# Performance work log

Measured on AMD Instinct MI355X. Metric: run time of the kernel, lower is better.

## Reference

```python
import jax, jax.numpy as jnp
import numpy as np

V, E, H = 50000, 300, 512            # vocab, embed dim, rnn hidden
BS, NSEG, SLEN = 64, 3, 256          # batch, segments per sample (hardcoded 3), max seg len
NNODE, NFEAT, NHID, NOUT = 18, 600, 600, 1024  # GCN dims (hardcoded in module)


def _uniform(k, shape, stdv):
    return jax.random.uniform(k, shape, jnp.float32, -stdv, stdv)


def setup_inputs() -> dict:
    key = jax.random.key(0)
    ks = jax.random.split(key, 14)
    input_inds = jax.random.randint(ks[0], (BS, NSEG, SLEN), 0, V, dtype=jnp.int32)
    input_lens = jax.random.randint(ks[1], (BS, NSEG), 1, SLEN + 1, dtype=jnp.int32)
    emb = jax.random.normal(ks[2], (V, E), jnp.float32) * 0.1
    # GRU params (torch layout: [3H, in])
    sx = float(np.sqrt(6.0 / (3 * H + E)))
    sh = float(np.sqrt(6.0 / (3 * H + H)))
    w_ih = _uniform(ks[3], (3 * H, E), sx)
    w_hh = _uniform(ks[4], (3 * H, H), sh)
    b_ih = jnp.zeros((3 * H,), jnp.float32)
    b_hh = jnp.zeros((3 * H,), jnp.float32)
    # GCN params (uniform +-1/sqrt(out_features), per reset_parameters)
    s1 = 1.0 / float(np.sqrt(NHID))
    s2 = 1.0 / float(np.sqrt(NOUT))
    gw1 = _uniform(ks[5], (NFEAT, NHID), s1)
    gb1 = _uniform(ks[6], (NHID,), s1)
    gw2 = _uniform(ks[7], (NHID, NOUT), s2)
    gb2 = _uniform(ks[8], (NOUT,), s2)
    sg_x = jax.random.normal(ks[9], (BS, NNODE, NFEAT), jnp.float32)
    adj = jax.random.uniform(ks[10], (BS, NNODE, NNODE), jnp.float32)
    return dict(input_inds=input_inds, input_lens=input_lens, emb=emb,
                w_ih=w_ih, w_hh=w_hh, b_ih=b_ih, b_hh=b_hh,
                sg_x=sg_x, adj=adj, gw1=gw1, gb1=gb1, gw2=gw2, gb2=gb2)


def _gru(x, lens, w_ih, w_hh, b_ih, b_hh):
    """Length-masked batched GRU. x: [B,T,E], lens: [B]. Returns ys [B,T,H], hT [B,H]
    where hT equals the hidden state at the last valid step (carry frozen after len)."""
    B, T, _ = x.shape
    Hh = w_hh.shape[1]
    xi = jnp.einsum('bte,ge->btg', x, w_ih) + b_ih  # precompute input gates [B,T,3H]

    def step(h, inp):
        xi_t, t = inp
        gh = h @ w_hh.T + b_hh
        xr, xz, xn = jnp.split(xi_t, 3, axis=-1)
        hr, hz, hn = jnp.split(gh, 3, axis=-1)
        r = jax.nn.sigmoid(xr + hr)
        z = jax.nn.sigmoid(xz + hz)
        n = jnp.tanh(xn + r * hn)
        h_new = (1.0 - z) * n + z * h
        h_out = jnp.where((t < lens)[:, None], h_new, h)
        return h_out, h_out

    h0 = jnp.zeros((B, Hh), x.dtype)
    hT, ys = jax.lax.scan(step, h0, (jnp.swapaxes(xi, 0, 1), jnp.arange(T)))
    return jnp.swapaxes(ys, 0, 1), hT


def reference(input_inds, input_lens, emb, w_ih, w_hh, b_ih, b_hh,
              sg_x, adj, gw1, gb1, gw2, gb2):
    B3 = BS * NSEG
    T = NSEG * SLEN
    tok = emb[input_inds.reshape(B3, SLEN)]           # [B3, SLEN, E]
    ys, hT = _gru(tok, input_lens.reshape(B3), w_ih, w_hh, b_ih, b_hh)

    # Pack valid (segment, t) outputs contiguously per sample (the torch cat of
    # per-segment ragged outputs), pad tail with zeros.
    lens = input_lens                                            # [BS, NSEG]
    offs = jnp.concatenate([jnp.zeros((BS, 1), jnp.int32),
                            jnp.cumsum(lens, axis=1)[:, :-1]], axis=1)
    t_idx = jnp.arange(SLEN, dtype=jnp.int32)
    valid = t_idx[None, None, :] < lens[:, :, None]              # [BS, NSEG, SLEN]
    pos = jnp.where(valid, offs[:, :, None] + t_idx[None, None, :], T)
    pos = pos.reshape(BS, T)
    b_ix = jnp.arange(BS)[:, None]
    out_rfts = jnp.zeros((BS, T + 1, H), ys.dtype).at[b_ix, pos].set(
        ys.reshape(BS, T, H))[:, :T]
    out_embs = jnp.zeros((BS, T + 1, E), tok.dtype).at[b_ix, pos].set(
        tok.reshape(BS, T, E))[:, :T]
    tlen = jnp.sum(lens, axis=1)
    out_msks = (jnp.arange(T)[None, :] < tlen[:, None]).astype(jnp.float32)
    out_hids = hT.reshape(BS, NSEG, H)                           # final h per segment

    # GCN: relu(adj @ (x W1) + b1); adj @ (h W2) + b2
    h1 = jax.nn.relu(jnp.einsum('bnm,bmf->bnf', adj, sg_x @ gw1) + gb1)
    out_sg = jnp.einsum('bnm,bmf->bnf', adj, h1 @ gw2) + gb2
    return out_rfts, out_embs, out_msks, out_sg, out_hids
```

## Files before the change

### kernel.cpp

```cpp
#include <hip/hip_runtime.h>


typedef unsigned short ushort_t;
typedef __attribute__((ext_vector_type(8))) short bf16x8;
typedef __attribute__((ext_vector_type(4))) float f32x4;

#define OUT_RFTS 0UL
#define OUT_EMBS 25165824UL
#define OUT_MSKS 39911424UL
#define OUT_SG   39960576UL
#define OUT_HIDS 41140224UL

#define WS_HX   0UL
#define WS_FLG  393216UL

__device__ __forceinline__ ushort_t f2b(float f) {
  unsigned int u = __float_as_uint(f);
  u += 0x7fffu + ((u >> 16) & 1u);
  return (ushort_t)(u >> 16);
}

union FRAG { ushort_t s[8]; bf16x8 v; uint2 u2[2]; };

__device__ __forceinline__ bf16x8 frag_from_f32(const float* p, bool v0, bool v1) {
  float4 a = v0 ? *(const float4*)p       : make_float4(0.f, 0.f, 0.f, 0.f);
  float4 b = v1 ? *(const float4*)(p + 4) : make_float4(0.f, 0.f, 0.f, 0.f);
  FRAG u;
  u.s[0] = f2b(a.x); u.s[1] = f2b(a.y); u.s[2] = f2b(a.z); u.s[3] = f2b(a.w);
  u.s[4] = f2b(b.x); u.s[5] = f2b(b.y); u.s[6] = f2b(b.z); u.s[7] = f2b(b.w);
  return u.v;
}

__global__ __launch_bounds__(256, 1) void fused_all(
    const int* __restrict__ inds, const int* __restrict__ lens,
    const float* __restrict__ emb, const float* __restrict__ w_ih,
    const float* __restrict__ w_hh, const float* __restrict__ b_ih,
    const float* __restrict__ b_hh,
    const float* __restrict__ sgx, const float* __restrict__ adj,
    const float* __restrict__ gw1, const float* __restrict__ gb1,
    const float* __restrict__ gw2, const float* __restrict__ gb2,
    ushort_t* __restrict__ hx, unsigned int* __restrict__ flags,
    float* __restrict__ out)
{
  __shared__ __attribute__((aligned(16))) char smem[92304];
  const int bid = blockIdx.x;
  const int tid = threadIdx.x;

  if (bid < 96) {
    ushort_t* hst = (ushort_t*)smem;
    ushort_t (*tokb)[16 * 328] = (ushort_t (*)[16 * 328])(smem + 16640);
    int* sidx = (int*)(smem + 37632);

    const int g = bid >> 3;
    const int p = bid & 7;
    const int w = tid >> 6;
    const int l = tid & 63;
    const int jc = l & 15;
    const int quad = l >> 4;
    const int jg = p * 64 + w * 16 + jc;

    bf16x8 bwh[3][16];
#pragma unroll
    for (int g3 = 0; g3 < 3; ++g3) {
      const float* wr = w_hh + (size_t)(g3 * 512 + jg) * 512 + quad * 8;
#pragma unroll
      for (int kc = 0; kc < 16; ++kc)
        bwh[g3][kc] = frag_from_f32(wr + kc * 32, true, true);
    }
    bf16x8 bwx[3][10];
#pragma unroll
    for (int g3 = 0; g3 < 3; ++g3) {
      const float* wr = w_ih + (size_t)(g3 * 512 + jg) * 300;
#pragma unroll
      for (int kc = 0; kc < 10; ++kc) {
        const int k0 = kc * 32 + quad * 8;
        bwx[g3][kc] = frag_from_f32(wr + k0, k0 + 3 < 300, k0 + 7 < 300);
      }
    }
    const float bsr = b_ih[jg] + b_hh[jg];
    const float bsz = b_ih[512 + jg] + b_hh[512 + jg];
    const float bin = b_ih[1024 + jg];
    const float bhn = b_hh[1024 + jg];

    int Tg = 0;
    for (int i = 0; i < 16; ++i) Tg = max(Tg, lens[g * 16 + i]);

    int len_q[4]; size_t rf_q[4], hxo_q[4], hid_q[4];
    float h_q[4] = {0.f, 0.f, 0.f, 0.f};
#pragma unroll
    for (int q = 0; q < 4; ++q) {
      int sl = quad * 4 + q;
      int b3 = g * 16 + sl;
      len_q[q] = lens[b3];
      int b = b3 / 3, seg = b3 - b * 3;
      int off = 0;
      for (int ss = 0; ss < seg; ++ss) off += lens[b * 3 + ss];
      rf_q[q]  = OUT_RFTS + ((size_t)b * 768 + off) * 512 + jg;
      hxo_q[q] = (size_t)b3 * 512 + (size_t)(jg & ~1);
      hid_q[q] = OUT_HIDS + (size_t)b3 * 512 + jg;
    }

    int trow[5], tcu[5];
#pragma unroll
    for (int c = 0; c < 5; ++c) {
      int u = c * 256 + tid;
      trow[c] = u / 80;
      tcu[c]  = u - trow[c] * 80;
    }

    if (tid < 16) sidx[tid] = inds[(size_t)(g * 16 + tid) * 256 + 0];
    __syncthreads();
#pragma unroll
    for (int c = 0; c < 5; ++c) {
      float4 v = make_float4(0.f, 0.f, 0.f, 0.f);
      if (tcu[c] < 75)
        v = *(const float4*)(emb + (size_t)sidx[trow[c]] * 300 + tcu[c] * 4);
      FRAG u; u.s[0] = f2b(v.x); u.s[1] = f2b(v.y); u.s[2] = f2b(v.z); u.s[3] = f2b(v.w);
      *(uint2*)(&tokb[0][trow[c] * 328 + tcu[c] * 4]) = u.u2[0];
    }
    __syncthreads();

    const int HXE = 192 * 512;
    const f32x4 z4 = {0.f, 0.f, 0.f, 0.f};

    for (int t = 0; t < Tg; ++t) {
      const int buf = t & 1, nbuf = buf ^ 1;
      if (tid < 8) {
        long guard = 0;
        while (__hip_atomic_load(&flags[(g * 8 + tid) * 32],
                                 __ATOMIC_RELAXED, __HIP_MEMORY_SCOPE_AGENT)
               < (unsigned int)t) {
          __builtin_amdgcn_s_sleep(1);
          if (++guard > 20000000L) break;
        }
      }
      if (tid < 64) __builtin_amdgcn_fence(__ATOMIC_ACQUIRE, "agent");
      if (tid < 16) {
        int tt = (t + 1 < 256) ? t + 1 : 255;
        sidx[tid] = inds[(size_t)(g * 16 + tid) * 256 + tt];
      }
      __syncthreads();
      {
        const unsigned long long* src =
            (const unsigned long long*)(hx + (size_t)buf * HXE + (size_t)g * 16 * 512);
#pragma unroll
        for (int c = 0; c < 8; ++c) {
          int idx = c * 256 + tid;
          unsigned long long v = __hip_atomic_load(
              (unsigned long long*)(src + idx), __ATOMIC_RELAXED, __HIP_MEMORY_SCOPE_AGENT);
          int row = idx >> 7, col = idx & 127;
          *(unsigned long long*)(&hst[row * 520 + col * 4]) = v;
        }
      }
      __syncthreads();
      float4 tr[5];
#pragma unroll
      for (int c = 0; c < 5; ++c) {
        tr[c] = make_float4(0.f, 0.f, 0.f, 0.f);
        if (tcu[c] < 75)
          tr[c] = *(const float4*)(emb + (size_t)sidx[trow[c]] * 300 + tcu[c] * 4);
      }
      f32x4 accr = z4, accz = z4, anh = z4, anx = z4;
#pragma unroll
      for (int kc = 0; kc < 16; ++kc) {
        bf16x8 af = *(const bf16x8*)(&hst[(l & 15) * 520 + kc * 32 + quad * 8]);
        accr = __builtin_amdgcn_mfma_f32_16x16x32_bf16(af, bwh[0][kc], accr, 0, 0, 0);
        accz = __builtin_amdgcn_mfma_f32_16x16x32_bf16(af, bwh[1][kc], accz, 0, 0, 0);
        anh  = __builtin_amdgcn_mfma_f32_16x16x32_bf16(af, bwh[2][kc], anh, 0, 0, 0);
      }
#pragma unroll
      for (int kc = 0; kc < 10; ++kc) {
        bf16x8 xf = *(const bf16x8*)(&tokb[buf][(l & 15) * 328 + kc * 32 + quad * 8]);
        accr = __builtin_amdgcn_mfma_f32_16x16x32_bf16(xf, bwx[0][kc], accr, 0, 0, 0);
        accz = __builtin_amdgcn_mfma_f32_16x16x32_bf16(xf, bwx[1][kc], accz, 0, 0, 0);
        anx  = __builtin_amdgcn_mfma_f32_16x16x32_bf16(xf, bwx[2][kc], anx, 0, 0, 0);
      }
      ushort_t* hxout = hx + (size_t)nbuf * HXE;
#pragma unroll
      for (int q = 0; q < 4; ++q) {
        float pr = accr[q] + bsr;
        float pz = accz[q] + bsz;
        float r = 1.f / (1.f + __expf(-pr));
        float z = 1.f / (1.f + __expf(-pz));
        float e2 = __expf(2.f * (anx[q] + bin + r * (anh[q] + bhn)));
        float n = 1.f - 2.f / (e2 + 1.f);
        float hn = (1.f - z) * n + z * h_q[q];
        bool valid = (t < len_q[q]);
        hn = valid ? hn : h_q[q];
        h_q[q] = hn;
        if (valid) out[rf_q[q] + (size_t)t * 512] = hn;
        unsigned int hb = f2b(hn);
        unsigned int ob = (unsigned int)__shfl_xor((int)hb, 1, 64) & 0xffffu;
        if ((jc & 1) == 0) {
          unsigned int pv = (hb & 0xffffu) | (ob << 16);
          __hip_atomic_store((unsigned int*)(hxout + hxo_q[q]), pv,
                             __ATOMIC_RELAXED, __HIP_MEMORY_SCOPE_AGENT);
        }
      }
#pragma unroll
      for (int c = 0; c < 5; ++c) {
        FRAG u;
        u.s[0] = f2b(tr[c].x); u.s[1] = f2b(tr[c].y);
        u.s[2] = f2b(tr[c].z); u.s[3] = f2b(tr[c].w);
        *(uint2*)(&tokb[nbuf][trow[c] * 328 + tcu[c] * 4]) = u.u2[0];
      }
      __syncthreads();
      if (tid == 0)
        __hip_atomic_store(&flags[(g * 8 + p) * 32], (unsigned int)(t + 1),
                           __ATOMIC_RELAXED, __HIP_MEMORY_SCOPE_AGENT);
    }
#pragma unroll
    for (int q = 0; q < 4; ++q) out[hid_q[q]] = h_q[q];

  } else if (bid < 160) {
    const int b = bid - 96;
    float* xs   = (float*)smem;
    float* h1s  = (float*)smem + 10800;
    float* adjs = (float*)smem + 21600;
    float* ts   = (float*)smem + 21924;

    for (int i = tid; i < 18 * 600; i += 256) xs[i] = sgx[(size_t)b * 10800 + i];
    for (int i = tid; i < 324; i += 256) adjs[i] = adj[(size_t)b * 324 + i];
    __syncthreads();

    for (int cb = 0; cb < 10; ++cb) {
      const int c0 = cb * 64;
      for (int o = tid; o < 1152; o += 256) {
        const int r = o >> 6, c = c0 + (o & 63);
        float a0 = 0.f, a1 = 0.f;
        if (c < 600) {
          const float* xr = xs + r * 600;
          for (int k = 0; k < 600; k += 2) {
            a0 += xr[k]     * gw1[(size_t)k * 600 + c];
            a1 += xr[k + 1] * gw1[(size_t)(k + 1) * 600 + c];
          }
        }
        ts[o] = a0 + a1;
      }
      __syncthreads();
      for (int o = tid; o < 1152; o += 256) {
        const int n = o >> 6, cl = o & 63, c = c0 + cl;
        if (c < 600) {
          float acc = gb1[c];
#pragma unroll
          for (int m = 0; m < 18; ++m) acc += adjs[n * 18 + m] * ts[m * 64 + cl];
          h1s[n * 600 + c] = fmaxf(acc, 0.f);
        }
      }
      __syncthreads();
    }
    for (int cb = 0; cb < 16; ++cb) {
      const int c0 = cb * 64;
      for (int o = tid; o < 1152; o += 256) {
        const int r = o >> 6, c = c0 + (o & 63);
        const float* xr = h1s + r * 600;
        float a0 = 0.f, a1 = 0.f;
        for (int k = 0; k < 600; k += 2) {
          a0 += xr[k]     * gw2[(size_t)k * 1024 + c];
          a1 += xr[k + 1] * gw2[(size_t)(k + 1) * 1024 + c];
        }
        ts[o] = a0 + a1;
      }
      __syncthreads();
      for (int o = tid; o < 1152; o += 256) {
        const int n = o >> 6, cl = o & 63, c = c0 + cl;
        float acc = gb2[c];
#pragma unroll
        for (int m = 0; m < 18; ++m) acc += adjs[n * 18 + m] * ts[m * 64 + cl];
        out[OUT_SG + (size_t)b * 18432 + n * 1024 + c] = acc;
      }
      __syncthreads();
    }

  } else {
    const int wid = (bid - 160) * 4 + (tid >> 6);
    const int l = tid & 63;
    for (int j = 0; j < 128; ++j) {
      const int pr = wid + 384 * j;
      const int b = pr / 768;
      const int p = pr - b * 768;
      const int l0 = lens[b * 3], l1 = lens[b * 3 + 1], l2 = lens[b * 3 + 2];
      const int tlen = l0 + l1 + l2;
      if (l == 0)
        out[OUT_MSKS + (size_t)b * 768 + p] = (p < tlen) ? 1.0f : 0.0f;
      const size_t rfoff = OUT_RFTS + ((size_t)b * 768 + p) * 512;
      const size_t eboff = OUT_EMBS + ((size_t)b * 768 + p) * 300;
      if (p >= tlen) {
        const float4 z4 = make_float4(0.f, 0.f, 0.f, 0.f);
        *(float4*)(out + rfoff + (size_t)l * 8)     = z4;
        *(float4*)(out + rfoff + (size_t)l * 8 + 4) = z4;
        for (int u = l; u < 75; u += 64)
          *(float4*)(out + eboff + (size_t)u * 4) = z4;
      } else {
        int s, tt;
        if (p < l0)           { s = 0; tt = p; }
        else if (p < l0 + l1) { s = 1; tt = p - l0; }
        else                  { s = 2; tt = p - l0 - l1; }
        const int ind = inds[(b * 3 + s) * 256 + tt];
        const float* src = emb + (size_t)ind * 300;
        for (int u = l; u < 75; u += 64)
          *(float4*)(out + eboff + (size_t)u * 4) = *(const float4*)(src + (size_t)u * 4);
      }
    }
  }
}

extern "C" void kernel_launch(void* const* d_in, const int* in_sizes, int n_in,
                              void* d_out, int out_size, void* d_ws, size_t ws_size,
                              hipStream_t stream)
{
  (void)in_sizes; (void)n_in; (void)out_size; (void)ws_size;
  const int*   inds = (const int*)d_in[0];
  const int*   lens = (const int*)d_in[1];
  const float* emb  = (const float*)d_in[2];
  const float* w_ih = (const float*)d_in[3];
  const float* w_hh = (const float*)d_in[4];
  const float* b_ih = (const float*)d_in[5];
  const float* b_hh = (const float*)d_in[6];
  const float* sgx  = (const float*)d_in[7];
  const float* adj  = (const float*)d_in[8];
  const float* gw1  = (const float*)d_in[9];
  const float* gb1  = (const float*)d_in[10];
  const float* gw2  = (const float*)d_in[11];
  const float* gb2  = (const float*)d_in[12];
  float* out = (float*)d_out;
  char* ws = (char*)d_ws;
  ushort_t* hx = (ushort_t*)(ws + WS_HX);
  unsigned int* flags = (unsigned int*)(ws + WS_FLG);

  hipMemsetAsync(ws, 0, 405504, stream);
  fused_all<<<dim3(256), 256, 0, stream>>>(inds, lens, emb, w_ih, w_hh, b_ih, b_hh,
                                           sgx, adj, gw1, gb1, gw2, gb2,
                                           hx, flags, out);
}
```

Measured before the change: 1.878 ms.

## Interleave two GRU groups per block and use cache-bypassing hidden-state exchange

Each recurrent block now handles two batch groups in alternation, which halves the recurrent block count from 96 to 48 and frees blocks for the mask/embedding copy work (now 144 blocks, stride 576). Hidden-state exchange uses inline-asm sc0 sc1 loads and stores with an explicit vmcnt wait instead of relaxed atomics plus an acquire fence. The flag is now published before the output stores, so the global ys writes leave the critical path. The aim is to hide each group's inter-block spin-wait latency behind the other group's compute. The cost is doubled serial work per block, and correctness now relies on the asm cache bits giving coherence without a fence.

```diff
diff --git a/kernel.cpp b/kernel.cpp
--- a/kernel.cpp
+++ b/kernel.cpp
@@ -4,6 +4,7 @@
 typedef unsigned short ushort_t;
 typedef __attribute__((ext_vector_type(8))) short bf16x8;
 typedef __attribute__((ext_vector_type(4))) float f32x4;
+typedef __attribute__((ext_vector_type(4))) unsigned int u32x4;
 
 #define OUT_RFTS 0UL
 #define OUT_EMBS 25165824UL
@@ -29,6 +30,22 @@
   u.s[0] = f2b(a.x); u.s[1] = f2b(a.y); u.s[2] = f2b(a.z); u.s[3] = f2b(a.w);
   u.s[4] = f2b(b.x); u.s[5] = f2b(b.y); u.s[6] = f2b(b.z); u.s[7] = f2b(b.w);
   return u.v;
+}
+
+__device__ __forceinline__ void st_mall_u32(void* a, unsigned int v) {
+  asm volatile("global_store_dword %0, %1, off sc0 sc1" :: "v"(a), "v"(v) : "memory");
+}
+__device__ __forceinline__ void ld4x16_mall(
+    const char* a0, const char* a1, const char* a2, const char* a3,
+    u32x4& v0, u32x4& v1, u32x4& v2, u32x4& v3) {
+  asm volatile(
+      "global_load_dwordx4 %0, %4, off sc0 sc1\n\t"
+      "global_load_dwordx4 %1, %5, off sc0 sc1\n\t"
+      "global_load_dwordx4 %2, %6, off sc0 sc1\n\t"
+      "global_load_dwordx4 %3, %7, off sc0 sc1\n\t"
+      "s_waitcnt vmcnt(0)"
+      : "=&v"(v0), "=&v"(v1), "=&v"(v2), "=&v"(v3)
+      : "v"(a0), "v"(a1), "v"(a2), "v"(a3) : "memory");
 }
 
 __global__ __launch_bounds__(256, 1) void fused_all(
@@ -46,18 +63,25 @@
   const int bid = blockIdx.x;
   const int tid = threadIdx.x;
 
-  if (bid < 96) {
-    ushort_t* hst = (ushort_t*)smem;
-    ushort_t (*tokb)[16 * 328] = (ushort_t (*)[16 * 328])(smem + 16640);
-    int* sidx = (int*)(smem + 37632);
-
-    const int g = bid >> 3;
-    const int p = bid & 7;
+  if (bid < 48) {
+    const int gp = bid >> 3;
+    const int p  = bid & 7;
+    const int gA = gp * 2, gB = gp * 2 + 1;
+
+    ushort_t* hstA = (ushort_t*)smem;
+    ushort_t* hstB = (ushort_t*)(smem + 16640);
+    ushort_t* tokA = (ushort_t*)(smem + 33280);
+    ushort_t* tokB = (ushort_t*)(smem + 54272);
+    int* sidxA = (int*)(smem + 75264);
+    int* sidxB = (int*)(smem + 75328);
+
     const int w = tid >> 6;
     const int l = tid & 63;
     const int jc = l & 15;
     const int quad = l >> 4;
     const int jg = p * 64 + w * 16 + jc;
+    const int flA = (gA * 8 + p) * 32;
+    const int flB = (gB * 8 + p) * 32;
 
     bf16x8 bwh[3][16];
 #pragma unroll
@@ -82,23 +106,34 @@
     const float bin = b_ih[1024 + jg];
     const float bhn = b_hh[1024 + jg];
 
-    int Tg = 0;
-    for (int i = 0; i < 16; ++i) Tg = max(Tg, lens[g * 16 + i]);
-
-    int len_q[4]; size_t rf_q[4], hxo_q[4], hid_q[4];
-    float h_q[4] = {0.f, 0.f, 0.f, 0.f};
-#pragma unroll
-    for (int q = 0; q < 4; ++q) {
-      int sl = quad * 4 + q;
-      int b3 = g * 16 + sl;
-      len_q[q] = lens[b3];
-      int b = b3 / 3, seg = b3 - b * 3;
-      int off = 0;
-      for (int ss = 0; ss < seg; ++ss) off += lens[b * 3 + ss];
-      rf_q[q]  = OUT_RFTS + ((size_t)b * 768 + off) * 512 + jg;
-      hxo_q[q] = (size_t)b3 * 512 + (size_t)(jg & ~1);
-      hid_q[q] = OUT_HIDS + (size_t)b3 * 512 + jg;
-    }
+    int TgA = 0, TgB = 0;
+    for (int i = 0; i < 16; ++i) {
+      TgA = max(TgA, lens[gA * 16 + i]);
+      TgB = max(TgB, lens[gB * 16 + i]);
+    }
+
+    int lenA[4], lenB[4];
+    unsigned int rfA[4], rfB[4], hxoA[4], hxoB[4], hidA[4], hidB[4];
+    float hA[4] = {0.f, 0.f, 0.f, 0.f};
+    float hB[4] = {0.f, 0.f, 0.f, 0.f};
+
+    auto setup = [&](int g, int* len_q, unsigned int* rf_q,
+                     unsigned int* hxo_q, unsigned int* hid_q) {
+#pragma unroll
+      for (int q = 0; q < 4; ++q) {
+        int sl = quad * 4 + q;
+        int b3 = g * 16 + sl;
+        len_q[q] = lens[b3];
+        int b = b3 / 3, seg = b3 - b * 3;
+        int off = 0;
+        for (int ss = 0; ss < seg; ++ss) off += lens[b * 3 + ss];
+        rf_q[q]  = (unsigned int)(((unsigned)b * 768u + (unsigned)off) * 512u + (unsigned)jg);
+        hxo_q[q] = (unsigned int)(b3 * 512 + (jg & ~1));
+        hid_q[q] = (unsigned int)(OUT_HIDS + (size_t)b3 * 512 + jg);
+      }
+    };
+    setup(gA, lenA, rfA, hxoA, hidA);
+    setup(gB, lenB, rfB, hxoB, hidB);
 
     int trow[5], tcu[5];
 #pragma unroll
@@ -108,49 +143,60 @@
       tcu[c]  = u - trow[c] * 80;
     }
 
-    if (tid < 16) sidx[tid] = inds[(size_t)(g * 16 + tid) * 256 + 0];
+    if (tid < 16) {
+      sidxA[tid] = inds[(size_t)(gA * 16 + tid) * 256 + 0];
+      sidxB[tid] = inds[(size_t)(gB * 16 + tid) * 256 + 0];
+    }
     __syncthreads();
 #pragma unroll
     for (int c = 0; c < 5; ++c) {
-      float4 v = make_float4(0.f, 0.f, 0.f, 0.f);
-      if (tcu[c] < 75)
-        v = *(const float4*)(emb + (size_t)sidx[trow[c]] * 300 + tcu[c] * 4);
-      FRAG u; u.s[0] = f2b(v.x); u.s[1] = f2b(v.y); u.s[2] = f2b(v.z); u.s[3] = f2b(v.w);
-      *(uint2*)(&tokb[0][trow[c] * 328 + tcu[c] * 4]) = u.u2[0];
+      float4 va = make_float4(0.f, 0.f, 0.f, 0.f);
+      float4 vb = make_float4(0.f, 0.f, 0.f, 0.f);
+      if (tcu[c] < 75) {
+        va = *(const float4*)(emb + (size_t)sidxA[trow[c]] * 300 + tcu[c] * 4);
+        vb = *(const float4*)(emb + (size_t)sidxB[trow[c]] * 300 + tcu[c] * 4);
+      }
+      FRAG ua, ub;
+      ua.s[0] = f2b(va.x); ua.s[1] = f2b(va.y); ua.s[2] = f2b(va.z); ua.s[3] = f2b(va.w);
+      ub.s[0] = f2b(vb.x); ub.s[1] = f2b(vb.y); ub.s[2] = f2b(vb.z); ub.s[3] = f2b(vb.w);
+      *(uint2*)(&tokA[trow[c] * 328 + tcu[c] * 4]) = ua.u2[0];
+      *(uint2*)(&tokB[trow[c] * 328 + tcu[c] * 4]) = ub.u2[0];
     }
     __syncthreads();
 
     const int HXE = 192 * 512;
     const f32x4 z4 = {0.f, 0.f, 0.f, 0.f};
 
-    for (int t = 0; t < Tg; ++t) {
-      const int buf = t & 1, nbuf = buf ^ 1;
-      if (tid < 8) {
+    auto gstep = [&](int g, int fl, int t, int buf, int nbuf,
+                     ushort_t* hst, ushort_t* tokbase, int* sidx,
+                     float* h_q, int* len_q, unsigned int* rf_q,
+                     unsigned int* hxo_q) {
+      if (l < 8) {
+        const unsigned int* fa = &flags[(g * 8 + l) * 32];
         long guard = 0;
-        while (__hip_atomic_load(&flags[(g * 8 + tid) * 32],
-                                 __ATOMIC_RELAXED, __HIP_MEMORY_SCOPE_AGENT)
+        while (__hip_atomic_load(fa, __ATOMIC_RELAXED, __HIP_MEMORY_SCOPE_AGENT)
                < (unsigned int)t) {
           __builtin_amdgcn_s_sleep(1);
-          if (++guard > 20000000L) break;
-        }
-      }
-      if (tid < 64) __builtin_amdgcn_fence(__ATOMIC_ACQUIRE, "agent");
+          if (++guard > 5000000L) break;
+        }
+      }
       if (tid < 16) {
         int tt = (t + 1 < 256) ? t + 1 : 255;
         sidx[tid] = inds[(size_t)(g * 16 + tid) * 256 + tt];
       }
-      __syncthreads();
       {
-        const unsigned long long* src =
-            (const unsigned long long*)(hx + (size_t)buf * HXE + (size_t)g * 16 * 512);
-#pragma unroll
-        for (int c = 0; c < 8; ++c) {
-          int idx = c * 256 + tid;
-          unsigned long long v = __hip_atomic_load(
-              (unsigned long long*)(src + idx), __ATOMIC_RELAXED, __HIP_MEMORY_SCOPE_AGENT);
-          int row = idx >> 7, col = idx & 127;
-          *(unsigned long long*)(&hst[row * 520 + col * 4]) = v;
-        }
+        const char* hsrc = (const char*)(hx + (size_t)buf * HXE + (size_t)g * 16 * 512);
+        u32x4 v0, v1, v2, v3;
+        ld4x16_mall(hsrc + (size_t)(0 * 256 + tid) * 16,
+                    hsrc + (size_t)(1 * 256 + tid) * 16,
+                    hsrc + (size_t)(2 * 256 + tid) * 16,
+                    hsrc + (size_t)(3 * 256 + tid) * 16,
+                    v0, v1, v2, v3);
+        const int i0 = tid, i1 = 256 + tid, i2 = 512 + tid, i3 = 768 + tid;
+        *(u32x4*)(&hst[(i0 >> 6) * 520 + (i0 & 63) * 8]) = v0;
+        *(u32x4*)(&hst[(i1 >> 6) * 520 + (i1 & 63) * 8]) = v1;
+        *(u32x4*)(&hst[(i2 >> 6) * 520 + (i2 & 63) * 8]) = v2;
+        *(u32x4*)(&hst[(i3 >> 6) * 520 + (i3 & 63) * 8]) = v3;
       }
       __syncthreads();
       float4 tr[5];
@@ -161,6 +207,7 @@
           tr[c] = *(const float4*)(emb + (size_t)sidx[trow[c]] * 300 + tcu[c] * 4);
       }
       f32x4 accr = z4, accz = z4, anh = z4, anx = z4;
+      const ushort_t* tokc = tokbase + buf * (16 * 328);
 #pragma unroll
       for (int kc = 0; kc < 16; ++kc) {
         bf16x8 af = *(const bf16x8*)(&hst[(l & 15) * 520 + kc * 32 + quad * 8]);
@@ -170,7 +217,7 @@
       }
 #pragma unroll
       for (int kc = 0; kc < 10; ++kc) {
-        bf16x8 xf = *(const bf16x8*)(&tokb[buf][(l & 15) * 328 + kc * 32 + quad * 8]);
+        bf16x8 xf = *(const bf16x8*)(&tokc[(l & 15) * 328 + kc * 32 + quad * 8]);
         accr = __builtin_amdgcn_mfma_f32_16x16x32_bf16(xf, bwx[0][kc], accr, 0, 0, 0);
         accz = __builtin_amdgcn_mfma_f32_16x16x32_bf16(xf, bwx[1][kc], accz, 0, 0, 0);
         anx  = __builtin_amdgcn_mfma_f32_16x16x32_bf16(xf, bwx[2][kc], anx, 0, 0, 0);
@@ -185,35 +232,47 @@
         float e2 = __expf(2.f * (anx[q] + bin + r * (anh[q] + bhn)));
         float n = 1.f - 2.f / (e2 + 1.f);
         float hn = (1.f - z) * n + z * h_q[q];
-        bool valid = (t < len_q[q]);
-        hn = valid ? hn : h_q[q];
+        hn = (t < len_q[q]) ? hn : h_q[q];
         h_q[q] = hn;
-        if (valid) out[rf_q[q] + (size_t)t * 512] = hn;
         unsigned int hb = f2b(hn);
         unsigned int ob = (unsigned int)__shfl_xor((int)hb, 1, 64) & 0xffffu;
         if ((jc & 1) == 0) {
           unsigned int pv = (hb & 0xffffu) | (ob << 16);
-          __hip_atomic_store((unsigned int*)(hxout + hxo_q[q]), pv,
-                             __ATOMIC_RELAXED, __HIP_MEMORY_SCOPE_AGENT);
-        }
-      }
+          st_mall_u32((void*)(hxout + hxo_q[q]), pv);
+        }
+      }
+      asm volatile("s_waitcnt vmcnt(0)" ::: "memory");
+      __syncthreads();
+      if (tid == 0)
+        __hip_atomic_store(&flags[fl], (unsigned int)(t + 1),
+                           __ATOMIC_RELAXED, __HIP_MEMORY_SCOPE_AGENT);
+#pragma unroll
+      for (int q = 0; q < 4; ++q)
+        if (t < len_q[q]) out[(size_t)rf_q[q] + (size_t)t * 512] = h_q[q];
+      ushort_t* tokn = tokbase + nbuf * (16 * 328);
 #pragma unroll
       for (int c = 0; c < 5; ++c) {
         FRAG u;
         u.s[0] = f2b(tr[c].x); u.s[1] = f2b(tr[c].y);
         u.s[2] = f2b(tr[c].z); u.s[3] = f2b(tr[c].w);
-        *(uint2*)(&tokb[nbuf][trow[c] * 328 + tcu[c] * 4]) = u.u2[0];
-      }
-      __syncthreads();
-      if (tid == 0)
-        __hip_atomic_store(&flags[(g * 8 + p) * 32], (unsigned int)(t + 1),
-                           __ATOMIC_RELAXED, __HIP_MEMORY_SCOPE_AGENT);
-    }
-#pragma unroll
-    for (int q = 0; q < 4; ++q) out[hid_q[q]] = h_q[q];
-
-  } else if (bid < 160) {
-    const int b = bid - 96;
+        *(uint2*)(&tokn[trow[c] * 328 + tcu[c] * 4]) = u.u2[0];
+      }
+    };
+
+    const int Tmax = max(TgA, TgB);
+    for (int t = 0; t < Tmax; ++t) {
+      const int buf = t & 1, nbuf = buf ^ 1;
+      if (t < TgA) gstep(gA, flA, t, buf, nbuf, hstA, tokA, sidxA, hA, lenA, rfA, hxoA);
+      if (t < TgB) gstep(gB, flB, t, buf, nbuf, hstB, tokB, sidxB, hB, lenB, rfB, hxoB);
+    }
+#pragma unroll
+    for (int q = 0; q < 4; ++q) {
+      out[hidA[q]] = hA[q];
+      out[hidB[q]] = hB[q];
+    }
+
+  } else if (bid < 112) {
+    const int b = bid - 48;
     float* xs   = (float*)smem;
     float* h1s  = (float*)smem + 10800;
     float* adjs = (float*)smem + 21600;
@@ -273,30 +332,29 @@
     }
 
   } else {
-    const int wid = (bid - 160) * 4 + (tid >> 6);
+    const int wid = (bid - 112) * 4 + (tid >> 6);
     const int l = tid & 63;
-    for (int j = 0; j < 128; ++j) {
-      const int pr = wid + 384 * j;
+    for (int pr = wid; pr < 49152; pr += 576) {
       const int b = pr / 768;
-      const int p = pr - b * 768;
-      const int l0 = lens[b * 3], l1 = lens[b * 3 + 1], l2 = lens[b * 3 + 2];
-      const int tlen = l0 + l1 + l2;
+      const int pp = pr - b * 768;
+      const int l0 = lens[b * 3], l1 = lens[b * 3 + 1], l2v = lens[b * 3 + 2];
+      const int tlen = l0 + l1 + l2v;
       if (l == 0)
-        out[OUT_MSKS + (size_t)b * 768 + p] = (p < tlen) ? 1.0f : 0.0f;
-      const size_t rfoff = OUT_RFTS + ((size_t)b * 768 + p) * 512;
-      const size_t eboff = OUT_EMBS + ((size_t)b * 768 + p) * 300;
-      if (p >= tlen) {
-        const float4 z4 = make_float4(0.f, 0.f, 0.f, 0.f);
-        *(float4*)(out + rfoff + (size_t)l * 8)     = z4;
-        *(float4*)(out + rfoff + (size_t)l * 8 + 4) = z4;
+        out[OUT_MSKS + (size_t)b * 768 + pp] = (pp < tlen) ? 1.0f : 0.0f;
+      const size_t rfoff = OUT_RFTS + ((size_t)b * 768 + pp) * 512;
+      const size_t eboff = OUT_EMBS + ((size_t)b * 768 + pp) * 300;
+      if (pp >= tlen) {
+        const float4 zz = make_float4(0.f, 0.f, 0.f, 0.f);
+        *(float4*)(out + rfoff + (size_t)l * 8)     = zz;
+        *(float4*)(out + rfoff + (size_t)l * 8 + 4) = zz;
         for (int u = l; u < 75; u += 64)
-          *(float4*)(out + eboff + (size_t)u * 4) = z4;
+          *(float4*)(out + eboff + (size_t)u * 4) = zz;
       } else {
-        int s, tt;
-        if (p < l0)           { s = 0; tt = p; }
-        else if (p < l0 + l1) { s = 1; tt = p - l0; }
-        else                  { s = 2; tt = p - l0 - l1; }
-        const int ind = inds[(b * 3 + s) * 256 + tt];
+        int sgi, tt;
+        if (pp < l0)           { sgi = 0; tt = pp; }
+        else if (pp < l0 + l1) { sgi = 1; tt = pp - l0; }
+        else                   { sgi = 2; tt = pp - l0 - l1; }
+        const int ind = inds[(b * 3 + sgi) * 256 + tt];
         const float* src = emb + (size_t)ind * 300;
         for (int u = l; u < 75; u += 64)
           *(float4*)(out + eboff + (size_t)u * 4) = *(const float4*)(src + (size_t)u * 4);
```

After: 3.354 ms. 78.5% more time.
